# Performance work log

Measured on AMD Instinct MI355X. Metric: run time of the kernel, lower is better.

The kernel has to match this reference:

```python
import jax, jax.numpy as jnp
import numpy as np


def _lstm_cell(x, h, c, W_ih, W_hh, b_ih, b_hh):
    # PyTorch LSTM cell, gate order (i, f, g, o)
    gates = x @ W_ih.T + b_ih + h @ W_hh.T + b_hh
    i, f, g, o = jnp.split(gates, 4, axis=-1)
    c = jax.nn.sigmoid(f) * c + jax.nn.sigmoid(i) * jnp.tanh(g)
    h = jax.nn.sigmoid(o) * jnp.tanh(c)
    return h, c


def setup_inputs() -> dict:
    key = jax.random.key(0)
    B, T, F, H = 512, 256, 128, 512
    ks = jax.random.split(key, 12)
    s = 1.0 / np.sqrt(H)  # PyTorch-style uniform-ish scale (use scaled normal)
    inp = {
        'ts_batch': jax.random.normal(ks[0], (B, T, F), jnp.float32),
        'enc_W_ih': jax.random.normal(ks[1], (4 * H, F), jnp.float32) * s,
        'enc_W_hh': jax.random.normal(ks[2], (4 * H, H), jnp.float32) * s,
        'enc_b_ih': jax.random.normal(ks[3], (4 * H,), jnp.float32) * s,
        'enc_b_hh': jax.random.normal(ks[4], (4 * H,), jnp.float32) * s,
        'dec_W_ih': jax.random.normal(ks[5], (4 * H, F), jnp.float32) * s,
        'dec_W_hh': jax.random.normal(ks[6], (4 * H, H), jnp.float32) * s,
        'dec_b_ih': jax.random.normal(ks[7], (4 * H,), jnp.float32) * s,
        'dec_b_hh': jax.random.normal(ks[8], (4 * H,), jnp.float32) * s,
        'Wo': jax.random.normal(ks[9], (F, H), jnp.float32) * s,
        'bo': jax.random.normal(ks[10], (F,), jnp.float32) * s,
    }
    return inp


def reference(ts_batch, enc_W_ih, enc_W_hh, enc_b_ih, enc_b_hh,
              dec_W_ih, dec_W_hh, dec_b_ih, dec_b_hh, Wo, bo):
    B, T, F = ts_batch.shape
    H = enc_W_hh.shape[1]
    dt = ts_batch.dtype
    h0 = jnp.zeros((B, H), dt)
    c0 = jnp.zeros((B, H), dt)

    # --- encoder: standard LSTM over time, keep final hidden state ---
    def enc_step(carry, x_t):
        h, c = carry
        h, c = _lstm_cell(x_t, h, c, enc_W_ih, enc_W_hh, enc_b_ih, enc_b_hh)
        return (h, c), None

    xs = jnp.swapaxes(ts_batch, 0, 1)  # [T, B, F]
    (h_enc, _), _ = jax.lax.scan(enc_step, (h0, c0), xs)

    # --- decoder: free-running (eval mode), iterating i = T-1 .. 0 ---
    # at each step: emit y = Linear(h), then feed y through decoder LSTM
    def dec_step(carry, _):
        h, c = carry
        y = h @ Wo.T + bo  # [B, F]
        h, c = _lstm_cell(y, h, c, dec_W_ih, dec_W_hh, dec_b_ih, dec_b_hh)
        return (h, c), y

    _, ys = jax.lax.scan(dec_step, (h_enc, c0), None, length=T)  # [T, B, F]
    # ys[0] corresponds to output[:, T-1], ys[T-1] to output[:, 0] -> flip
    output = jnp.flip(jnp.swapaxes(ys, 0, 1), axis=1)  # [B, T, F]
    return output
```

## Files before the change

### kernel.cpp

```cpp
#include <hip/hip_runtime.h>

#define Bn 512
#define Tn 256
#define Fn 128
#define Hn 512
#define KIE32 40
#define KID32 32
#define EH 20
#define DH 16
#define KID 16
#define NWG 256
#define RS 648

typedef __attribute__((ext_vector_type(8))) __bf16 bf16x8;
typedef __attribute__((ext_vector_type(4))) float floatx4;
typedef __attribute__((ext_vector_type(16))) float floatx16;
typedef __attribute__((ext_vector_type(4))) unsigned uintx4;

__device__ __forceinline__ unsigned short f2bf_u16(float f) {
  union { float f; unsigned u; } v; v.f = f;
  unsigned r = v.u + 0x7FFFu + ((v.u >> 16) & 1u);
  return (unsigned short)(r >> 16);
}

__device__ __forceinline__ float sigm(float x) {
  return __builtin_amdgcn_rcpf(1.f + __expf(-x));
}
__device__ __forceinline__ float ftanh(float x) {
  return 1.f - 2.f * __builtin_amdgcn_rcpf(1.f + __expf(2.f * x));
}

__global__ void pack_enc_k(const float* __restrict__ Wih, const float* __restrict__ Whh,
                           unsigned short* __restrict__ Bpe) {
  int id = blockIdx.x;
  int nt = id / KIE32, ki = id % KIE32;
  int l = threadIdx.x;
  int n = nt * 32 + (l & 31);
  int kb = ki * 16 + (l >> 5) * 8;
  __align__(16) unsigned short o[8];
#pragma unroll
  for (int j = 0; j < 8; ++j) {
    int k = kb + j;
    float v = (k < Fn) ? Wih[n * Fn + k] : Whh[n * Hn + (k - Fn)];
    o[j] = f2bf_u16(v);
  }
  *(uint4*)(Bpe + (size_t)(id * 64 + l) * 8) = *(uint4*)o;
}

__global__ void pack_dec_k(const float* __restrict__ Wih, const float* __restrict__ Whh,
                           const float* __restrict__ Wo, unsigned short* __restrict__ Bpd) {
  int id = blockIdx.x;
  int nt = id / KID32, ki = id % KID32;
  int l = threadIdx.x;
  int n = nt * 32 + (l & 31);
  int kb = ki * 16 + (l >> 5) * 8;
  float acc[8];
#pragma unroll
  for (int j = 0; j < 8; ++j) acc[j] = Whh[n * Hn + kb + j];
  for (int f = 0; f < Fn; ++f) {
    float wf = Wih[n * Fn + f];
    const float* wo = Wo + f * Hn + kb;
#pragma unroll
    for (int j = 0; j < 8; ++j) acc[j] += wf * wo[j];
  }
  __align__(16) unsigned short o[8];
#pragma unroll
  for (int j = 0; j < 8; ++j) o[j] = f2bf_u16(acc[j]);
  *(uint4*)(Bpd + (size_t)(id * 64 + l) * 8) = *(uint4*)o;
}

__global__ void pack_wo_k(const float* __restrict__ Wo, unsigned short* __restrict__ Bpw) {
  int id = blockIdx.x;
  int ft = id / KID, ki = id % KID;
  int l = threadIdx.x;
  int f = ft * 16 + (l & 15);
  int kb = ki * 32 + (l >> 4) * 8;
  __align__(16) unsigned short o[8];
#pragma unroll
  for (int j = 0; j < 8; ++j) o[j] = f2bf_u16(Wo[f * Hn + kb + j]);
  *(uint4*)(Bpw + (size_t)(id * 64 + l) * 8) = *(uint4*)o;
}

__global__ void bias_k(const float* __restrict__ ebih, const float* __restrict__ ebhh,
                       const float* __restrict__ dbih, const float* __restrict__ dbhh,
                       const float* __restrict__ dWih, const float* __restrict__ bo,
                       float* __restrict__ benc, float* __restrict__ bdec) {
  int n = blockIdx.x * blockDim.x + threadIdx.x;
  benc[n] = ebih[n] + ebhh[n];
  float a = dbih[n] + dbhh[n];
  for (int f = 0; f < Fn; ++f) a += dWih[n * Fn + f] * bo[f];
  bdec[n] = a;
}

__global__ void pack_x_k(const float* __restrict__ ts, unsigned short* __restrict__ xp) {
  size_t i = (size_t)blockIdx.x * 256 + threadIdx.x;
  int k4 = (int)(i & 31);
  size_t bs = i >> 5;
  int s = (int)(bs & 255);
  size_t b = bs >> 8;
  float4 v = *(const float4*)(ts + (i << 2));
  __align__(8) unsigned short o[4];
  o[0] = f2bf_u16(v.x); o[1] = f2bf_u16(v.y); o[2] = f2bf_u16(v.z); o[3] = f2bf_u16(v.w);
  *(unsigned long long*)(xp + ((size_t)s * Bn + b) * Fn + k4 * 4) = *(unsigned long long*)o;
}

__global__ void init_k(unsigned long long* __restrict__ Hg0,
                       unsigned* __restrict__ flgA, unsigned* __restrict__ flgB,
                       unsigned* __restrict__ xcdP) {
  int i = blockIdx.x * 256 + threadIdx.x;
  Hg0[i] = 0ULL;
  if (i < 8192) { flgA[i] = 0u; flgB[i] = 0u; }
  if (i < NWG) xcdP[i] = 0xFFu;
}

#define POLL(F, p) do { \
  if (l < 16) { \
    const unsigned* fp_ = (F) + (size_t)(mg * 16 + l) * 32; \
    while (__hip_atomic_load(fp_, __ATOMIC_RELAXED, __HIP_MEMORY_SCOPE_AGENT) < (unsigned)(p)) \
      __builtin_amdgcn_s_sleep(1); \
  } \
  __asm__ __volatile__("" ::: "memory"); \
} while (0)

#define SETF(F, p) do { if (tid == 0) \
  __hip_atomic_store((F) + (size_t)gid * 32, (unsigned)(p), __ATOMIC_RELAXED, __HIP_MEMORY_SCOPE_AGENT); \
} while (0)

#define STAGE_H2(OFF, curbuf) do { \
  const unsigned short* sp_ = Hg + (size_t)(curbuf) * (Bn * Hn) + (size_t)(b0 + sh_r) * Hn + sh_c * 32; \
  uintx4 t0_, t1_, t2_, t3_; \
  if (loc) { \
    asm volatile("global_load_dwordx4 %0, %4, off sc0\n\t" \
                 "global_load_dwordx4 %1, %4, off offset:16 sc0\n\t" \
                 "global_load_dwordx4 %2, %4, off offset:32 sc0\n\t" \
                 "global_load_dwordx4 %3, %4, off offset:48 sc0\n\t" \
                 "s_waitcnt vmcnt(0)" \
                 : "=&v"(t0_), "=&v"(t1_), "=&v"(t2_), "=&v"(t3_) : "v"(sp_) : "memory"); \
  } else { \
    const unsigned long long* src_ = (const unsigned long long*)sp_; \
    unsigned long long v_[8]; \
    _Pragma("unroll") for (int u_ = 0; u_ < 8; ++u_) \
      v_[u_] = __hip_atomic_load(src_ + u_, __ATOMIC_RELAXED, __HIP_MEMORY_SCOPE_AGENT); \
    t0_[0] = (unsigned)v_[0]; t0_[1] = (unsigned)(v_[0] >> 32); t0_[2] = (unsigned)v_[1]; t0_[3] = (unsigned)(v_[1] >> 32); \
    t1_[0] = (unsigned)v_[2]; t1_[1] = (unsigned)(v_[2] >> 32); t1_[2] = (unsigned)v_[3]; t1_[3] = (unsigned)(v_[3] >> 32); \
    t2_[0] = (unsigned)v_[4]; t2_[1] = (unsigned)(v_[4] >> 32); t2_[2] = (unsigned)v_[5]; t2_[3] = (unsigned)(v_[5] >> 32); \
    t3_[0] = (unsigned)v_[6]; t3_[1] = (unsigned)(v_[6] >> 32); t3_[2] = (unsigned)v_[7]; t3_[3] = (unsigned)(v_[7] >> 32); \
  } \
  uintx4* dst_ = (uintx4*)&A_lds[sh_r * RS + (OFF) + sh_c * 32]; \
  dst_[0] = t0_; dst_[1] = t1_; dst_[2] = t2_; dst_[3] = t3_; \
} while (0)

#define STAGE_X2(s_) do { \
  uint4 xv_ = *(const uint4*)(xp + ((size_t)(s_) * Bn + b0 + sh_r) * Fn + sh_c * 8); \
  *(uint4*)&A_lds[sh_r * RS + sh_c * 8] = xv_; \
} while (0)

#define MFMA_Y(sd) do { \
  floatx4 ay_ = {0.f, 0.f, 0.f, 0.f}; \
  const unsigned short* Ay_ = &A_lds[(l15 + yro) * RS + q * 8]; \
  _Pragma("unroll") for (int k = 0; k < KID; ++k) \
    ay_ = __builtin_amdgcn_mfma_f32_16x16x32_bf16( \
        *(const bf16x8*)(Ay_ + k * 32), *(const bf16x8*)&Bw_lds[(k * 64 + l) * 8], ay_, 0, 0, 0); \
  _Pragma("unroll") for (int r = 0; r < 4; ++r) \
    __builtin_nontemporal_store(ay_[r] + bof, \
      out + ((size_t)(b0 + yro + q * 4 + r) * Tn + (Tn - 1 - (sd))) * Fn + ns * 16 + l15); \
} while (0)

#define GATES32(BR, KN, DOY, sd) do { \
  floatx16 a_ = {0.f}; \
  const unsigned short* Ar_ = &A_lds[l31 * RS + (kh * (KN)) * 16 + ksub]; \
  _Pragma("unroll") for (int t = 0; t < (KN); ++t) \
    a_ = __builtin_amdgcn_mfma_f32_32x32x16_bf16(*(const bf16x8*)(Ar_ + t * 16), (BR)[t], a_, 0, 0, 0); \
  if (kh) { \
    _Pragma("unroll") for (int r = 0; r < 16; ++r) \
      gates_lds[g2][(r & 3) + 8 * (r >> 2) + 4 * lhi][l31] = a_[r]; \
  } \
  if (DOY) MFMA_Y(sd); \
  __syncthreads(); \
  if (!kh) { \
    _Pragma("unroll") for (int r = 0; r < 16; ++r) { \
      int row_ = (r & 3) + 8 * (r >> 2) + 4 * lhi; \
      gates_lds[g2][row_][l31] += a_[r]; \
    } \
  } \
} while (0)

#define EPI2(BI, BF, BG, BO, nxtbuf) do { \
  float gi0_ = gates_lds[0][eb][ej] + (BI); \
  float gf0_ = gates_lds[1][eb][ej] + (BF); \
  float gg0_ = gates_lds[2][eb][ej] + (BG); \
  float go0_ = gates_lds[3][eb][ej] + (BO); \
  float gi1_ = gates_lds[0][eb + 16][ej] + (BI); \
  float gf1_ = gates_lds[1][eb + 16][ej] + (BF); \
  float gg1_ = gates_lds[2][eb + 16][ej] + (BG); \
  float go1_ = gates_lds[3][eb + 16][ej] + (BO); \
  cA = sigm(gf0_) * cA + sigm(gi0_) * ftanh(gg0_); \
  float h0_ = sigm(go0_) * ftanh(cA); \
  cB = sigm(gf1_) * cB + sigm(gi1_) * ftanh(gg1_); \
  float h1_ = sigm(go1_) * ftanh(cB); \
  unsigned short hv0_ = f2bf_u16(h0_), hv1_ = f2bf_u16(h1_); \
  unsigned short* hp0_ = Hg + (size_t)(nxtbuf) * (Bn * Hn) + (size_t)(b0 + eb) * Hn + j0 + ej; \
  unsigned short* hp1_ = hp0_ + 16 * Hn; \
  if (loc) { *hp0_ = hv0_; *hp1_ = hv1_; } \
  else { \
    __hip_atomic_store(hp0_, hv0_, __ATOMIC_RELAXED, __HIP_MEMORY_SCOPE_AGENT); \
    __hip_atomic_store(hp1_, hv1_, __ATOMIC_RELAXED, __HIP_MEMORY_SCOPE_AGENT); \
  } \
} while (0)

__global__ __launch_bounds__(512, 2) void lstm_persist(
    const unsigned short* __restrict__ xp,
    const unsigned short* __restrict__ Bpe,
    const unsigned short* __restrict__ Bpd,
    const unsigned short* __restrict__ Bpw,
    const float* __restrict__ benc,
    const float* __restrict__ bdec,
    const float* __restrict__ bo,
    unsigned short* __restrict__ Hg,
    unsigned* __restrict__ flgA,
    unsigned* __restrict__ flgB,
    unsigned* __restrict__ xcdPub,
    float* __restrict__ out)
{
  const int wg = blockIdx.x;
  const int tid = threadIdx.x;
  const int w = tid >> 6, l = tid & 63;
  const int l15 = l & 15, q = l >> 4;
  const int l31 = l & 31, lhi = l >> 5;
  const int g2 = w & 3, kh = w >> 2;
  const int ksub = lhi * 8;
  const int eb = tid >> 5, ej = tid & 31;
  const int sh_r = tid >> 4, sh_c = tid & 15;

  const int grp = wg & 7, rank = wg >> 3;
  const int mg = grp * 2 + (rank >> 4);
  const int ns = rank & 15;
  const int gid = mg * 16 + ns;
  const int b0 = mg * 32, j0 = ns * 32;

  __shared__ __align__(16) unsigned short A_lds[32 * RS];
  __shared__ __align__(16) float gates_lds[4][32][33];
  __shared__ __align__(16) unsigned short Bw_lds[KID * 64 * 8];
  __shared__ int sh_asn[2];

  if (tid == 0) {
    unsigned x_;
    asm volatile("s_getreg_b32 %0, hwreg(HW_REG_XCC_ID)" : "=s"(x_));
    x_ &= 15u;
    sh_asn[1] = (int)x_;
    __hip_atomic_store(&xcdPub[wg], x_, __ATOMIC_RELAXED, __HIP_MEMORY_SCOPE_AGENT);
  }
  __syncthreads();
  const unsigned myx = (unsigned)sh_asn[1];
  if (tid < 64) {
    int ok = 1;
    if (tid < 16) {
      const int phys = grp + 8 * ((mg & 1) * 16 + tid);
      unsigned v_ = 0xFFu;
      for (int it = 0; it < 32768; ++it) {
        v_ = __hip_atomic_load(&xcdPub[phys], __ATOMIC_RELAXED, __HIP_MEMORY_SCOPE_AGENT);
        if (v_ != 0xFFu) break;
        __builtin_amdgcn_s_sleep(2);
      }
      ok = (v_ == myx) ? 1 : 0;
    }
    int all_ = __all(ok) ? 1 : 0;
    if (tid == 0) sh_asn[0] = all_;
  }
  __syncthreads();
  const int loc = sh_asn[0];

  bf16x8 Bq[EH], Bd[DH];
  const int nt32 = g2 * 16 + ns;
  {
    const bf16x8* p = (const bf16x8*)Bpe + ((size_t)nt32 * KIE32 + kh * EH) * 64 + l;
#pragma unroll
    for (int k = 0; k < EH; ++k) Bq[k] = p[k * 64];
  }
  {
    const bf16x8* p = (const bf16x8*)Bpd + ((size_t)nt32 * KID32 + kh * DH) * 64 + l;
#pragma unroll
    for (int k = 0; k < DH; ++k) Bd[k] = p[k * 64];
  }
  const float bie = benc[0 * Hn + j0 + ej], bfe = benc[1 * Hn + j0 + ej];
  const float bge = benc[2 * Hn + j0 + ej], boe = benc[3 * Hn + j0 + ej];
  const float bid = bdec[0 * Hn + j0 + ej], bfd = bdec[1 * Hn + j0 + ej];
  const float bgd = bdec[2 * Hn + j0 + ej], bod = bdec[3 * Hn + j0 + ej];

  if (ns < 8) {
    const uint4* src = (const uint4*)(Bpw + (size_t)ns * (KID * 64 * 8));
    uint4* dst = (uint4*)Bw_lds;
    dst[tid * 2] = src[tid * 2];
    dst[tid * 2 + 1] = src[tid * 2 + 1];
  }
  const bool doY = (ns < 8) && (g2 == 3);
  const int yro = kh ? 16 : 0;
  float bof = 0.f;
  if (doY) bof = bo[ns * 16 + l15];

  float cA = 0.f, cB = 0.f;

  __syncthreads();

  for (int s = 0; s < Tn; ++s) {
    const int cur = s & 1, nxt = cur ^ 1;
    POLL(flgA, s);
    STAGE_X2(s);
    STAGE_H2(Fn, cur);
    __syncthreads();
    GATES32(Bq, EH, false, 0);
    __syncthreads();
    EPI2(bie, bfe, bge, boe, nxt);
    __syncthreads();
    SETF(flgA, s + 1);
  }

  cA = 0.f; cB = 0.f;
  for (int sd = 0; sd < Tn; ++sd) {
    const int phg = Tn + sd;
    const int cur = phg & 1, nxt = cur ^ 1;
    POLL(flgA, phg);
    STAGE_H2(0, cur);
    __syncthreads();
    GATES32(Bd, DH, doY, sd);
    __syncthreads();
    EPI2(bid, bfd, bgd, bod, nxt);
    __syncthreads();
    SETF(flgA, phg + 1);
  }
}

extern "C" void kernel_launch(void* const* d_in, const int* in_sizes, int n_in,
                              void* d_out, int out_size, void* d_ws, size_t ws_size,
                              hipStream_t stream) {
  const float* ts   = (const float*)d_in[0];
  const float* eWih = (const float*)d_in[1];
  const float* eWhh = (const float*)d_in[2];
  const float* ebih = (const float*)d_in[3];
  const float* ebhh = (const float*)d_in[4];
  const float* dWih = (const float*)d_in[5];
  const float* dWhh = (const float*)d_in[6];
  const float* dbih = (const float*)d_in[7];
  const float* dbhh = (const float*)d_in[8];
  const float* Wo   = (const float*)d_in[9];
  const float* bo   = (const float*)d_in[10];
  float* outp = (float*)d_out;

  char* ws = (char*)d_ws;
  unsigned short* Bpe  = (unsigned short*)(ws);
  unsigned short* Bpd  = (unsigned short*)(ws + 2621440);
  unsigned short* Bpw  = (unsigned short*)(ws + 4718592);
  float*          benc = (float*)(ws + 4849664);
  float*          bdec = (float*)(ws + 4857856);
  unsigned short* Hg   = (unsigned short*)(ws + 4866048);
  unsigned*       flgA = (unsigned*)(ws + 5914624);
  unsigned*       flgB = (unsigned*)(ws + 5947392);
  unsigned short* xp   = (unsigned short*)(ws + 5980160);
  unsigned*       xcdP = (unsigned*)outp;

  pack_enc_k<<<64 * KIE32, 64, 0, stream>>>(eWih, eWhh, Bpe);
  pack_dec_k<<<64 * KID32, 64, 0, stream>>>(dWih, dWhh, Wo, Bpd);
  pack_wo_k<<<8 * KID, 64, 0, stream>>>(Wo, Bpw);
  bias_k<<<8, 256, 0, stream>>>(ebih, ebhh, dbih, dbhh, dWih, bo, benc, bdec);
  pack_x_k<<<16384, 256, 0, stream>>>(ts, xp);
  init_k<<<256, 256, 0, stream>>>((unsigned long long*)Hg, flgA, flgB, xcdP);

  lstm_persist<<<NWG, 512, 0, stream>>>(xp, Bpe, Bpd, Bpw, benc, bdec, bo, Hg,
                                        flgA, flgB, xcdP, outp);
}
```

Baseline: 1.742 ms.

## Split gate accumulators, drop intra-GATES barrier, prefetch x before poll

Each k-half now writes its partial gate sums to separate LDS buffers, and the epilogue adds them. This removes the extra __syncthreads and the read-modify-write pass inside the gate computation. The MFMA chains are split into two independent accumulators so consecutive MFMAs do not wait on each other. The x load for each step is issued before the cross-workgroup flag poll so its latency overlaps the wait. Launch bounds drop to one block per CU, which allows more registers per thread and doubles the gates LDS footprint.

```diff
diff --git a/kernel.cpp b/kernel.cpp
--- a/kernel.cpp
+++ b/kernel.cpp
@@ -150,50 +150,40 @@
   dst_[0] = t0_; dst_[1] = t1_; dst_[2] = t2_; dst_[3] = t3_; \
 } while (0)
 
-#define STAGE_X2(s_) do { \
-  uint4 xv_ = *(const uint4*)(xp + ((size_t)(s_) * Bn + b0 + sh_r) * Fn + sh_c * 8); \
-  *(uint4*)&A_lds[sh_r * RS + sh_c * 8] = xv_; \
-} while (0)
-
 #define MFMA_Y(sd) do { \
-  floatx4 ay_ = {0.f, 0.f, 0.f, 0.f}; \
+  floatx4 ay0_ = {0.f, 0.f, 0.f, 0.f}, ay1_ = {0.f, 0.f, 0.f, 0.f}; \
   const unsigned short* Ay_ = &A_lds[(l15 + yro) * RS + q * 8]; \
-  _Pragma("unroll") for (int k = 0; k < KID; ++k) \
-    ay_ = __builtin_amdgcn_mfma_f32_16x16x32_bf16( \
-        *(const bf16x8*)(Ay_ + k * 32), *(const bf16x8*)&Bw_lds[(k * 64 + l) * 8], ay_, 0, 0, 0); \
+  _Pragma("unroll") for (int k = 0; k < KID; k += 2) { \
+    ay0_ = __builtin_amdgcn_mfma_f32_16x16x32_bf16( \
+        *(const bf16x8*)(Ay_ + k * 32), *(const bf16x8*)&Bw_lds[(k * 64 + l) * 8], ay0_, 0, 0, 0); \
+    ay1_ = __builtin_amdgcn_mfma_f32_16x16x32_bf16( \
+        *(const bf16x8*)(Ay_ + (k + 1) * 32), *(const bf16x8*)&Bw_lds[((k + 1) * 64 + l) * 8], ay1_, 0, 0, 0); \
+  } \
   _Pragma("unroll") for (int r = 0; r < 4; ++r) \
-    __builtin_nontemporal_store(ay_[r] + bof, \
+    __builtin_nontemporal_store(ay0_[r] + ay1_[r] + bof, \
       out + ((size_t)(b0 + yro + q * 4 + r) * Tn + (Tn - 1 - (sd))) * Fn + ns * 16 + l15); \
 } while (0)
 
-#define GATES32(BR, KN, DOY, sd) do { \
-  floatx16 a_ = {0.f}; \
+#define GATES32(BR, KN) do { \
+  floatx16 aE_ = {0.f}, aO_ = {0.f}; \
   const unsigned short* Ar_ = &A_lds[l31 * RS + (kh * (KN)) * 16 + ksub]; \
-  _Pragma("unroll") for (int t = 0; t < (KN); ++t) \
-    a_ = __builtin_amdgcn_mfma_f32_32x32x16_bf16(*(const bf16x8*)(Ar_ + t * 16), (BR)[t], a_, 0, 0, 0); \
-  if (kh) { \
-    _Pragma("unroll") for (int r = 0; r < 16; ++r) \
-      gates_lds[g2][(r & 3) + 8 * (r >> 2) + 4 * lhi][l31] = a_[r]; \
-  } \
-  if (DOY) MFMA_Y(sd); \
-  __syncthreads(); \
-  if (!kh) { \
-    _Pragma("unroll") for (int r = 0; r < 16; ++r) { \
-      int row_ = (r & 3) + 8 * (r >> 2) + 4 * lhi; \
-      gates_lds[g2][row_][l31] += a_[r]; \
-    } \
-  } \
+  _Pragma("unroll") for (int t = 0; t < (KN); t += 2) { \
+    aE_ = __builtin_amdgcn_mfma_f32_32x32x16_bf16(*(const bf16x8*)(Ar_ + t * 16), (BR)[t], aE_, 0, 0, 0); \
+    aO_ = __builtin_amdgcn_mfma_f32_32x32x16_bf16(*(const bf16x8*)(Ar_ + (t + 1) * 16), (BR)[t + 1], aO_, 0, 0, 0); \
+  } \
+  _Pragma("unroll") for (int r = 0; r < 16; ++r) \
+    gates_lds[kh][g2][(r & 3) + 8 * (r >> 2) + 4 * lhi][l31] = aE_[r] + aO_[r]; \
 } while (0)
 
 #define EPI2(BI, BF, BG, BO, nxtbuf) do { \
-  float gi0_ = gates_lds[0][eb][ej] + (BI); \
-  float gf0_ = gates_lds[1][eb][ej] + (BF); \
-  float gg0_ = gates_lds[2][eb][ej] + (BG); \
-  float go0_ = gates_lds[3][eb][ej] + (BO); \
-  float gi1_ = gates_lds[0][eb + 16][ej] + (BI); \
-  float gf1_ = gates_lds[1][eb + 16][ej] + (BF); \
-  float gg1_ = gates_lds[2][eb + 16][ej] + (BG); \
-  float go1_ = gates_lds[3][eb + 16][ej] + (BO); \
+  float gi0_ = gates_lds[0][0][eb][ej] + gates_lds[1][0][eb][ej] + (BI); \
+  float gf0_ = gates_lds[0][1][eb][ej] + gates_lds[1][1][eb][ej] + (BF); \
+  float gg0_ = gates_lds[0][2][eb][ej] + gates_lds[1][2][eb][ej] + (BG); \
+  float go0_ = gates_lds[0][3][eb][ej] + gates_lds[1][3][eb][ej] + (BO); \
+  float gi1_ = gates_lds[0][0][eb + 16][ej] + gates_lds[1][0][eb + 16][ej] + (BI); \
+  float gf1_ = gates_lds[0][1][eb + 16][ej] + gates_lds[1][1][eb + 16][ej] + (BF); \
+  float gg1_ = gates_lds[0][2][eb + 16][ej] + gates_lds[1][2][eb + 16][ej] + (BG); \
+  float go1_ = gates_lds[0][3][eb + 16][ej] + gates_lds[1][3][eb + 16][ej] + (BO); \
   cA = sigm(gf0_) * cA + sigm(gi0_) * ftanh(gg0_); \
   float h0_ = sigm(go0_) * ftanh(cA); \
   cB = sigm(gf1_) * cB + sigm(gi1_) * ftanh(gg1_); \
@@ -208,7 +198,7 @@
   } \
 } while (0)
 
-__global__ __launch_bounds__(512, 2) void lstm_persist(
+__global__ __launch_bounds__(512, 1) void lstm_persist(
     const unsigned short* __restrict__ xp,
     const unsigned short* __restrict__ Bpe,
     const unsigned short* __restrict__ Bpd,
@@ -239,7 +229,7 @@
   const int b0 = mg * 32, j0 = ns * 32;
 
   __shared__ __align__(16) unsigned short A_lds[32 * RS];
-  __shared__ __align__(16) float gates_lds[4][32][33];
+  __shared__ __align__(16) float gates_lds[2][4][32][33];
   __shared__ __align__(16) unsigned short Bw_lds[KID * 64 * 8];
   __shared__ int sh_asn[2];
 
@@ -304,11 +294,12 @@
 
   for (int s = 0; s < Tn; ++s) {
     const int cur = s & 1, nxt = cur ^ 1;
+    uint4 xv_ = *(const uint4*)(xp + ((size_t)s * Bn + b0 + sh_r) * Fn + sh_c * 8);
     POLL(flgA, s);
-    STAGE_X2(s);
     STAGE_H2(Fn, cur);
-    __syncthreads();
-    GATES32(Bq, EH, false, 0);
+    *(uint4*)&A_lds[sh_r * RS + sh_c * 8] = xv_;
+    __syncthreads();
+    GATES32(Bq, EH);
     __syncthreads();
     EPI2(bie, bfe, bge, boe, nxt);
     __syncthreads();
@@ -322,7 +313,8 @@
     POLL(flgA, phg);
     STAGE_H2(0, cur);
     __syncthreads();
-    GATES32(Bd, DH, doY, sd);
+    GATES32(Bd, DH);
+    if (doY) MFMA_Y(sd);
     __syncthreads();
     EPI2(bid, bfd, bgd, bod, nxt);
     __syncthreads();
```

Measured after the change: 1.646 ms. 5.5% less time.
